# Kernel tuning notes

Measured on AMD Instinct MI355X. Metric: run time of the kernel, lower is better.

The kernel has to match this reference:

```python
import math
import jax, jax.numpy as jnp
import numpy as np

B, L, DIM, HEADS = 4, 2048, 1024, 8
HEAD = DIM // HEADS  # 128
SCALE_BASE = 512.0
EPS = 1e-5  # nn.GroupNorm default


def _xpos(x, downscale=False):
    # x: (..., L, dh). Faithful port of the RetNet XPOS (Jamie-Stirling impl).
    l, dh = x.shape[-2], x.shape[-1]
    half = dh // 2
    pos = jnp.arange(l, dtype=x.dtype)
    base = (jnp.arange(0, dh, 2, dtype=x.dtype) + 0.4 * dh) / (1.4 * dh)  # (half,)
    scale = base[None, :] ** (pos[:, None] / SCALE_BASE)                  # (L, half)
    inv_freq = 1.0 / (10000.0 ** (jnp.arange(half, dtype=x.dtype) / half))
    sinusoid = pos[:, None] * inv_freq[None, :]                           # (L, half)
    sin, cos = jnp.sin(sinusoid), jnp.cos(sinusoid)
    if downscale:
        scale = 1.0 / scale
    s = jnp.repeat(sin * scale, 2, axis=-1)  # duplicate_interleave -> (L, dh)
    c = jnp.repeat(cos * scale, 2, axis=-1)
    x1, x2 = x[..., ::2], x[..., 1::2]
    rot = jnp.stack([-x2, x1], axis=-1).reshape(x.shape)  # rotate_every_two
    return x * c + rot * s


def _decay_mask(l, gammas):
    # D[h, n, m] = gamma_h ** (n - m) for n >= m else 0
    n = jnp.arange(l)[:, None]
    m = jnp.arange(l)[None, :]
    lg = jnp.log(gammas)  # (h,)
    expo = (n - m).astype(jnp.float32)[None, :, :] * lg[:, None, None]
    return jnp.where((n >= m)[None], jnp.exp(expo), 0.0)  # (h, L, L)


def setup_inputs() -> dict:
    key = jax.random.key(0)
    ks = jax.random.split(key, 6)
    d = DIM
    return {
        "X": jax.random.normal(ks[0], (B, L, DIM), dtype=jnp.float32),
        "W_Q": jax.random.normal(ks[1], (HEADS, DIM, HEAD), dtype=jnp.float32) / d,
        "W_K": jax.random.normal(ks[2], (HEADS, DIM, HEAD), dtype=jnp.float32) / d,
        "W_V": jax.random.normal(ks[3], (HEADS, DIM, HEAD), dtype=jnp.float32) / d,
        "W_G": jax.random.normal(ks[4], (DIM, DIM), dtype=jnp.float32) / d,
        "W_O": jax.random.normal(ks[5], (DIM, DIM), dtype=jnp.float32) / d,
        "gn_weight": jnp.ones((DIM,), dtype=jnp.float32),
        "gn_bias": jnp.zeros((DIM,), dtype=jnp.float32),
    }


def reference(X, W_Q, W_K, W_V, W_G, W_O, gn_weight, gn_bias):
    b, l, d = X.shape
    h = W_Q.shape[0]
    # gammas = 1 - exp(linspace(log 1/32, log 1/512, heads))
    gammas = 1.0 - jnp.exp(jnp.linspace(math.log(1.0 / 32.0), math.log(1.0 / 512.0), h)).astype(jnp.float32)

    Q = jnp.einsum('bld,hde->bhle', X, W_Q)
    K = jnp.einsum('bld,hde->bhle', X, W_K)
    V = jnp.einsum('bld,hdv->bhlv', X, W_V)
    Q = _xpos(Q)
    K = _xpos(K, downscale=True)

    D = _decay_mask(l, gammas).astype(X.dtype)           # (h, L, L)
    scores = jnp.einsum('bhle,bhme->bhlm', Q, K) * D[None]
    Y = jnp.einsum('bhlm,bhmv->bhlv', scores, V)          # (b, h, L, head_v)

    # GroupNorm(heads, V) on rows of shape (V,): normalize per head group
    mean = Y.mean(axis=-1, keepdims=True)
    var = Y.var(axis=-1, keepdims=True)
    Yn = (Y - mean) * jax.lax.rsqrt(var + EPS)
    Yn = jnp.transpose(Yn, (0, 2, 1, 3)).reshape(b, l, -1)  # concat heads -> (b, L, V)
    Yn = Yn * gn_weight + gn_bias

    G = X @ W_G
    out = (G * jax.nn.sigmoid(G) * Yn) @ W_O  # swish gate then output proj
    return out
```

## Files before the change

kernel.cpp:

```cpp
#include <hip/hip_runtime.h>
#include <cmath>

#define BB 4
#define LL 2048
#define DD 1024
#define HH 8
#define MM (BB * LL)

struct Gammas { float lg2[8]; };
struct MMArgs { const ushort* Bt[4]; void* C[4]; void* C2[4]; int emode[4]; };

typedef __attribute__((ext_vector_type(8))) short bf16x8;
typedef __attribute__((ext_vector_type(4))) float f32x4;

__device__ __forceinline__ ushort f2bf(float f) {
    uint u = __builtin_bit_cast(uint, f);
    uint r = (u + 0x7fffu + ((u >> 16) & 1u)) >> 16;
    return (ushort)r;
}
__device__ __forceinline__ float bf2f(ushort h) {
    uint u = ((uint)h) << 16;
    return __builtin_bit_cast(float, u);
}
__device__ __forceinline__ void gload16(const void* g, void* l) {
    __builtin_amdgcn_global_load_lds((const __attribute__((address_space(1))) void*)g,
                                     (__attribute__((address_space(3))) void*)l, 16, 0, 0);
}

__global__ void xpos_table_kernel(float4* __restrict__ tbl) {
    int tid = blockIdx.x * blockDim.x + threadIdx.x;
    if (tid >= LL * 64) return;
    int l = tid >> 6, i = tid & 63;
    float inv = powf(10000.0f, -(float)i / 64.0f);
    float ang = (float)l * inv;
    float s = sinf(ang), c = cosf(ang);
    float base = (2.0f * (float)i + 51.2f) / 179.2f;
    float sc = powf(base, (float)l / 512.0f);
    tbl[tid] = make_float4(c * sc, s * sc, c / sc, s / sc);
}

__global__ __launch_bounds__(256) void cast_kernel(const float* __restrict__ X,
                                                   ushort* __restrict__ Xb) {
    int i = (blockIdx.x * 256 + threadIdx.x) * 4;
    float4 v = *(const float4*)&X[i];
    ushort4 o;
    o.x = f2bf(v.x); o.y = f2bf(v.y); o.z = f2bf(v.z); o.w = f2bf(v.w);
    *(ushort4*)&Xb[i] = o;
}

__global__ __launch_bounds__(256) void wtrans_kernel(const float* __restrict__ W,
                                                     ushort* __restrict__ Wt, int perhead) {
    __shared__ float T[64][68];
    const int k0 = blockIdx.y * 64, n0 = blockIdx.x * 64;
    const int t = threadIdx.x;
    for (int f = t; f < 64 * 16; f += 256) {
        int kk = f >> 4, s = f & 15;
        int n = n0 + s * 4;
        size_t src = perhead ? (size_t)(n >> 7) * 131072 + (size_t)(k0 + kk) * 128 + (n & 127)
                             : (size_t)(k0 + kk) * 1024 + n;
        *(float4*)&T[kk][s * 4] = *(const float4*)&W[src];
    }
    __syncthreads();
    for (int f = t; f < 64 * 8; f += 256) {
        int n = f >> 3, s = f & 7;
        __align__(16) ushort tmp[8];
        #pragma unroll
        for (int j = 0; j < 8; j++) tmp[j] = f2bf(T[s * 8 + j][n]);
        *(uint4*)&Wt[(size_t)(n0 + n) * 1024 + k0 + s * 8] = *(uint4*)tmp;
    }
}

__global__ __launch_bounds__(256, 4) void mm_kernel(
    const ushort* __restrict__ A, MMArgs args, const float4* __restrict__ tbl)
{
    __shared__ __align__(16) ushort As[2][128 * 32];
    __shared__ __align__(16) ushort Bs[2][128 * 32];
    const int t = threadIdx.x;
    const int w = t >> 6, lane = t & 63;
    const int ln = lane & 15, quad = lane >> 4;
    const int which = blockIdx.x >> 3;
    const ushort* Bt = args.Bt[which];
    void* Cv = args.C[which];
    void* Cv2 = args.C2[which];
    const int emode = args.emode[which];
    const int n0 = (blockIdx.x & 7) * 128, m0 = blockIdx.y * 128;
    const int wm = w & 1, wn = w >> 1;

    f32x4 acc[4][4];
    const f32x4 fzero = {0.f, 0.f, 0.f, 0.f};
    #pragma unroll
    for (int i = 0; i < 4; i++)
        #pragma unroll
        for (int j = 0; j < 4; j++) acc[i][j] = fzero;

    const int srow = w * 32 + (lane >> 2);
    const int scol = (lane & 3) * 8;
    const ushort* ga  = A  + (size_t)(m0 + srow) * 1024 + scol;
    const ushort* ga2 = ga + 16 * 1024;
    const ushort* gb  = Bt + (size_t)(n0 + srow) * 1024 + scol;
    const ushort* gb2 = gb + 16 * 1024;
    const int lo1 = (w * 32) * 32;
    const int lo2 = (w * 32 + 16) * 32;

    gload16(ga, &As[0][lo1]);
    gload16(ga2, &As[0][lo2]);
    gload16(gb, &Bs[0][lo1]);
    gload16(gb2, &Bs[0][lo2]);
    __syncthreads();

    for (int kt = 0; kt < 1024; kt += 32) {
        const int cur = (kt >> 5) & 1;
        if (kt < 1024 - 32) {
            const int nk = kt + 32;
            gload16(ga + nk, &As[cur ^ 1][lo1]);
            gload16(ga2 + nk, &As[cur ^ 1][lo2]);
            gload16(gb + nk, &Bs[cur ^ 1][lo1]);
            gload16(gb2 + nk, &Bs[cur ^ 1][lo2]);
        }
        bf16x8 am[4], bn[4];
        #pragma unroll
        for (int i = 0; i < 4; i++)
            am[i] = *(const bf16x8*)&As[cur][(wm * 64 + i * 16 + ln) * 32 + quad * 8];
        #pragma unroll
        for (int i = 0; i < 4; i++)
            bn[i] = *(const bf16x8*)&Bs[cur][(wn * 64 + i * 16 + ln) * 32 + quad * 8];
        #pragma unroll
        for (int mi = 0; mi < 4; mi++)
            #pragma unroll
            for (int ni = 0; ni < 4; ni++)
                acc[mi][ni] = __builtin_amdgcn_mfma_f32_16x16x32_bf16(
                    am[mi], bn[ni], acc[mi][ni], 0, 0, 0);
        __syncthreads();
    }

    #pragma unroll
    for (int mi = 0; mi < 4; mi++) {
        #pragma unroll
        for (int ni = 0; ni < 4; ni++) {
            const int row0 = m0 + wm * 64 + mi * 16 + quad * 4;
            const int e = wn * 64 + ni * 16 + ln;
            const int col = n0 + e;
            if (emode == 5) {
                const int b = row0 >> 11, l0 = row0 & (LL - 1);
                ushort4 pk;
                pk.x = f2bf(acc[mi][ni][0]); pk.y = f2bf(acc[mi][ni][1]);
                pk.z = f2bf(acc[mi][ni][2]); pk.w = f2bf(acc[mi][ni][3]);
                *(ushort4*)&((ushort*)Cv)[((size_t)(b * 1024 + col)) * 2048 + l0] = pk;
                continue;
            }
            float vv[4];
            #pragma unroll
            for (int r = 0; r < 4; r++) {
                float v = acc[mi][ni][r];
                if (emode == 1 || emode == 2 || emode == 6) {
                    float4 tt = tbl[(size_t)((row0 + r) & (LL - 1)) * 64 + (e >> 1)];
                    float cc = (emode == 1) ? tt.x : tt.z;
                    float ss = (emode == 1) ? tt.y : tt.w;
                    float partner = __shfl_xor(v, 1);
                    float rot = (e & 1) ? partner : -partner;
                    v = v * cc + rot * ss;
                } else if (emode == 3) {
                    v = v / (1.0f + expf(-v));
                }
                vv[r] = v;
                if (emode == 4)
                    ((float*)Cv)[(size_t)(row0 + r) * 1024 + col] = v;
                else
                    ((ushort*)Cv)[(size_t)(row0 + r) * 1024 + col] = f2bf(v);
            }
            if (emode == 6) {
                const int b = row0 >> 11, l0 = row0 & (LL - 1);
                ushort4 pk;
                pk.x = f2bf(vv[0]); pk.y = f2bf(vv[1]);
                pk.z = f2bf(vv[2]); pk.w = f2bf(vv[3]);
                *(ushort4*)&((ushort*)Cv2)[((size_t)(b * 1024 + col)) * 2048 + l0] = pk;
            }
        }
    }
}

__global__ __launch_bounds__(256) void state_kernel(
    const ushort* __restrict__ Ktb, const ushort* __restrict__ Vt,
    ushort* __restrict__ Sb, Gammas gp)
{
    __shared__ __align__(16) ushort shbuf[2 * 128 * 72];
    ushort* Ktl = shbuf;
    ushort* Vwl = shbuf + 128 * 72;

    const int t = threadIdx.x;
    const int w = t >> 6, lane = t & 63, ln = lane & 15, quad = lane >> 4;
    const int c = blockIdx.x, bh = blockIdx.y;
    const int b = bh >> 3, h = bh & 7;
    const float lg2 = gp.lg2[h];
    const size_t tbase = ((size_t)b * 1024 + h * 128) * 2048 + (size_t)c * 64;

    const int sr = t >> 1, soff = (t & 1) * 32;
    #pragma unroll
    for (int j = 0; j < 4; j++)
        *(uint4*)&Ktl[sr * 72 + soff + j * 8] =
            *(const uint4*)&Ktb[tbase + (size_t)sr * 2048 + soff + j * 8];
    #pragma unroll
    for (int j = 0; j < 4; j++) {
        uint4 raw = *(const uint4*)&Vt[tbase + (size_t)sr * 2048 + soff + j * 8];
        ushort* rp = (ushort*)&raw;
        __align__(16) ushort tmp[8];
        #pragma unroll
        for (int jj = 0; jj < 8; jj++) {
            int m = soff + j * 8 + jj;
            tmp[jj] = f2bf(bf2f(rp[jj]) * exp2f(lg2 * (float)(63 - m)));
        }
        *(uint4*)&Vwl[sr * 72 + soff + j * 8] = *(uint4*)tmp;
    }
    __syncthreads();

    const int wm = w & 1, wn = w >> 1;
    f32x4 acc[4][4];
    const f32x4 fzero = {0.f, 0.f, 0.f, 0.f};
    #pragma unroll
    for (int i = 0; i < 4; i++)
        #pragma unroll
        for (int j = 0; j < 4; j++) acc[i][j] = fzero;

    #pragma unroll
    for (int ks = 0; ks < 2; ks++) {
        bf16x8 am[4], bn[4];
        #pragma unroll
        for (int mi = 0; mi < 4; mi++)
            am[mi] = *(const bf16x8*)&Ktl[(wm * 64 + mi * 16 + ln) * 72 + ks * 32 + quad * 8];
        #pragma unroll
        for (int ni = 0; ni < 4; ni++)
            bn[ni] = *(const bf16x8*)&Vwl[(wn * 64 + ni * 16 + ln) * 72 + ks * 32 + quad * 8];
        #pragma unroll
        for (int mi = 0; mi < 4; mi++)
            #pragma unroll
            for (int ni = 0; ni < 4; ni++)
                acc[mi][ni] = __builtin_amdgcn_mfma_f32_16x16x32_bf16(
                    am[mi], bn[ni], acc[mi][ni], 0, 0, 0);
    }
    __syncthreads();

    ushort* Lsh = shbuf;
    #pragma unroll
    for (int mi = 0; mi < 4; mi++) {
        #pragma unroll
        for (int ni = 0; ni < 4; ni++) {
            const int d0 = wm * 64 + mi * 16 + quad * 4;
            const int v = wn * 64 + ni * 16 + ln;
            ushort4 pk;
            pk.x = f2bf(acc[mi][ni][0]); pk.y = f2bf(acc[mi][ni][1]);
            pk.z = f2bf(acc[mi][ni][2]); pk.w = f2bf(acc[mi][ni][3]);
            *(ushort4*)&Lsh[v * 136 + d0] = pk;
        }
    }
    __syncthreads();
    ushort* dst = Sb + (size_t)(bh * 32 + c) * 128 * 128;
    const int orow = t >> 1, ooff = (t & 1) * 64;
    #pragma unroll
    for (int j = 0; j < 8; j++)
        *(uint4*)&dst[(size_t)orow * 128 + ooff + j * 8] =
            *(uint4*)&Lsh[orow * 136 + ooff + j * 8];
}

__global__ __launch_bounds__(256) void scan_kernel(ushort* __restrict__ Sb, Gammas gp)
{
    const int t = threadIdx.x;
    const int vb = blockIdx.x, bh = blockIdx.y;
    const int h = bh & 7;
    const float g64 = exp2f(64.0f * gp.lg2[h]);
    const int v = vb * 16 + (t >> 4);
    const int d0 = (t & 15) * 8;

    float acc[8];
    #pragma unroll
    for (int j = 0; j < 8; j++) acc[j] = 0.f;

    for (int c = 1; c < 32; c++) {
        ushort* p = Sb + ((size_t)(bh * 32 + (c - 1)) * 128 + v) * 128 + d0;
        uint4 lv = *(const uint4*)p;
        ushort* lp = (ushort*)&lv;
        __align__(16) ushort o[8];
        #pragma unroll
        for (int j = 0; j < 8; j++) {
            acc[j] = g64 * acc[j] + bf2f(lp[j]);
            o[j] = f2bf(acc[j]);
        }
        *(uint4*)p = *(uint4*)o;
    }
}

__global__ __launch_bounds__(256) void ret2_kernel(
    const ushort* __restrict__ Qb, const ushort* __restrict__ Kb,
    const ushort* __restrict__ Vt, const ushort* __restrict__ Pt,
    const ushort* __restrict__ Gb,
    const float* __restrict__ gnw, const float* __restrict__ gnb,
    ushort* __restrict__ Z, Gammas gp)
{
    __shared__ __align__(16) ushort Ks[64 * 136];
    __shared__ __align__(16) ushort Vs[128 * 72];
    __shared__ __align__(16) ushort Ss[64 * 72];
    __shared__ __align__(16) ushort Ps[128 * 136];

    const int t = threadIdx.x;
    const int w = t >> 6, lane = t & 63, ln = lane & 15, quad = lane >> 4;
    const int c = blockIdx.x, bh = blockIdx.y;
    const int b = bh >> 3, h = bh & 7;
    const float lg2 = gp.lg2[h];
    const size_t qkbase = (size_t)b * LL * 1024 + (size_t)h * 128;
    const size_t vtbase = ((size_t)b * 1024 + h * 128) * 2048;
    const int n0 = c * 64;

    float dmk[4], drr[4];
    #pragma unroll
    for (int kt = 0; kt < 4; kt++)
        dmk[kt] = exp2f(-(float)(kt * 16 + quad * 4) * lg2);
    #pragma unroll
    for (int r = 0; r < 4; r++)
        drr[r] = exp2f(-(float)r * lg2);

    float gwv[8], gbv[8];
    #pragma unroll
    for (int vt = 0; vt < 8; vt++) {
        gwv[vt] = gnw[h * 128 + vt * 16 + ln];
        gbv[vt] = gnb[h * 128 + vt * 16 + ln];
    }

    const int krow = t >> 4, kc = (t & 15) * 8;
    const int vrow = t >> 3, vc = (t & 7) * 8;
    #pragma unroll
    for (int i = 0; i < 4; i++)
        *(uint4*)&Ks[(krow + i * 16) * 136 + kc] =
            *(const uint4*)&Kb[qkbase + (size_t)(n0 + krow + i * 16) * 1024 + kc];
    #pragma unroll
    for (int i = 0; i < 4; i++)
        *(uint4*)&Vs[(vrow + i * 32) * 72 + vc] =
            *(const uint4*)&Vt[vtbase + (size_t)(vrow + i * 32) * 2048 + n0 + vc];
    if (c > 0) {
        const ushort* psrc = Pt + (size_t)(bh * 32 + (c - 1)) * 128 * 128;
        const int pr = t >> 1, poff = (t & 1) * 64;
        #pragma unroll
        for (int j = 0; j < 8; j++)
            *(uint4*)&Ps[pr * 136 + poff + j * 8] =
                *(const uint4*)&psrc[(size_t)pr * 128 + poff + j * 8];
    }

    bf16x8 aq[4];
    #pragma unroll
    for (int ks = 0; ks < 4; ks++)
        aq[ks] = *(const bf16x8*)&Qb[qkbase + (size_t)(n0 + 16 * w + ln) * 1024
                                     + ks * 32 + quad * 8];
    f32x4 y[8];
    const f32x4 fzero = {0.f, 0.f, 0.f, 0.f};
    #pragma unroll
    for (int vt = 0; vt < 8; vt++) y[vt] = fzero;

    __syncthreads();

    if (c > 0) {
        #pragma unroll
        for (int ks = 0; ks < 4; ks++) {
            #pragma unroll
            for (int vt = 0; vt < 8; vt++) {
                bf16x8 bp = *(const bf16x8*)&Ps[(vt * 16 + ln) * 136 + ks * 32 + quad * 8];
                y[vt] = __builtin_amdgcn_mfma_f32_16x16x32_bf16(aq[ks], bp, y[vt], 0, 0, 0);
            }
        }
        #pragma unroll
        for (int rr = 0; rr < 4; rr++) {
            const float sc = exp2f(lg2 * (float)(16 * w + quad * 4 + rr + 1));
            #pragma unroll
            for (int vt = 0; vt < 8; vt++) y[vt][rr] *= sc;
        }
    }

    f32x4 s4[4];
    #pragma unroll
    for (int kt = 0; kt < 4; kt++) s4[kt] = fzero;
    #pragma unroll
    for (int ks = 0; ks < 4; ks++) {
        #pragma unroll
        for (int kt = 0; kt < 4; kt++) {
            bf16x8 bk = *(const bf16x8*)&Ks[(kt * 16 + ln) * 136 + ks * 32 + quad * 8];
            s4[kt] = __builtin_amdgcn_mfma_f32_16x16x32_bf16(bk, aq[ks], s4[kt], 0, 0, 0);
        }
    }
    const float dq = exp2f((float)(16 * w + ln) * lg2);
    #pragma unroll
    for (int kt = 0; kt < 4; kt++) {
        const float db = dq * dmk[kt];
        ushort4 pk;
        pk.x = f2bf((kt * 16 + quad * 4 + 0 <= 16 * w + ln) ? s4[kt][0] * db * drr[0] : 0.f);
        pk.y = f2bf((kt * 16 + quad * 4 + 1 <= 16 * w + ln) ? s4[kt][1] * db * drr[1] : 0.f);
        pk.z = f2bf((kt * 16 + quad * 4 + 2 <= 16 * w + ln) ? s4[kt][2] * db * drr[2] : 0.f);
        pk.w = f2bf((kt * 16 + quad * 4 + 3 <= 16 * w + ln) ? s4[kt][3] * db * drr[3] : 0.f);
        *(ushort4*)&Ss[(16 * w + ln) * 72 + kt * 16 + quad * 4] = pk;
    }
    #pragma unroll
    for (int ks2 = 0; ks2 < 2; ks2++) {
        bf16x8 as = *(const bf16x8*)&Ss[(16 * w + ln) * 72 + ks2 * 32 + quad * 8];
        #pragma unroll
        for (int vt = 0; vt < 8; vt++) {
            bf16x8 bv = *(const bf16x8*)&Vs[(vt * 16 + ln) * 72 + ks2 * 32 + quad * 8];
            y[vt] = __builtin_amdgcn_mfma_f32_16x16x32_bf16(as, bv, y[vt], 0, 0, 0);
        }
    }

    #pragma unroll
    for (int r = 0; r < 4; r++) {
        float s = 0.f, sq = 0.f;
        #pragma unroll
        for (int vt = 0; vt < 8; vt++) {
            float v = y[vt][r];
            s += v; sq += v * v;
        }
        #pragma unroll
        for (int off = 8; off >= 1; off >>= 1) {
            s  += __shfl_xor(s, off, 64);
            sq += __shfl_xor(sq, off, 64);
        }
        float mean = s * 0.0078125f;
        float var = sq * 0.0078125f - mean * mean;
        float rstd = rsqrtf(var + 1e-5f);
        const size_t row = (size_t)(b * LL + n0 + 16 * w + quad * 4 + r);
        #pragma unroll
        for (int vt = 0; vt < 8; vt++) {
            float gv = bf2f(Gb[row * 1024 + h * 128 + vt * 16 + ln]);
            float o = (y[vt][r] - mean) * rstd * gwv[vt] + gbv[vt];
            Z[row * 1024 + h * 128 + vt * 16 + ln] = f2bf(o * gv);
        }
    }
}

extern "C" void kernel_launch(void* const* d_in, const int* in_sizes, int n_in,
                              void* d_out, int out_size, void* d_ws, size_t ws_size,
                              hipStream_t stream) {
    const float* X   = (const float*)d_in[0];
    const float* Wq  = (const float*)d_in[1];
    const float* Wk  = (const float*)d_in[2];
    const float* Wv  = (const float*)d_in[3];
    const float* Wg  = (const float*)d_in[4];
    const float* Wo  = (const float*)d_in[5];
    const float* gnw = (const float*)d_in[6];
    const float* gnb = (const float*)d_in[7];
    float* out = (float*)d_out;

    const size_t MB = 1u << 20;
    char* base = (char*)d_ws;
    ushort* Sb  = (ushort*)base;
    float4* tbl = (float4*)base;
    ushort* Xb  = (ushort*)(base + 2 * MB);
    ushort* Wqt = (ushort*)(base + 18 * MB);
    ushort* Wkt = (ushort*)(base + 20 * MB);
    ushort* Wvt = (ushort*)(base + 22 * MB);
    ushort* Wgt = (ushort*)(base + 24 * MB);
    ushort* Wot = (ushort*)(base + 32 * MB);
    ushort* Qb  = (ushort*)(base + 34 * MB);
    ushort* Kb  = (ushort*)(base + 50 * MB);
    ushort* Gb  = (ushort*)(base + 66 * MB);
    ushort* Vt  = (ushort*)(base + 82 * MB);
    ushort* Ktb = (ushort*)(base + 98 * MB);
    ushort* Zb  = (ushort*)(base + 98 * MB);

    Gammas gp;
    for (int h = 0; h < 8; h++) {
        double lin = log(1.0 / 32.0) +
                     (log(1.0 / 512.0) - log(1.0 / 32.0)) * (double)h / 7.0;
        float gamma = 1.0f - expf((float)lin);
        gp.lg2[h] = log2f(gamma);
    }

    xpos_table_kernel<<<(LL * 64) / 256, 256, 0, stream>>>(tbl);
    cast_kernel<<<MM * 1024 / 1024, 256, 0, stream>>>(X, Xb);

    dim3 wgrid(16, 16);
    wtrans_kernel<<<wgrid, 256, 0, stream>>>(Wq, Wqt, 1);
    wtrans_kernel<<<wgrid, 256, 0, stream>>>(Wk, Wkt, 1);
    wtrans_kernel<<<wgrid, 256, 0, stream>>>(Wv, Wvt, 1);
    wtrans_kernel<<<wgrid, 256, 0, stream>>>(Wg, Wgt, 0);
    wtrans_kernel<<<wgrid, 256, 0, stream>>>(Wo, Wot, 0);

    MMArgs qa;
    qa.Bt[0] = Wqt; qa.Bt[1] = Wkt; qa.Bt[2] = Wvt; qa.Bt[3] = Wgt;
    qa.C[0] = Qb;   qa.C[1] = Kb;   qa.C[2] = Vt;   qa.C[3] = Gb;
    qa.C2[0] = nullptr; qa.C2[1] = Ktb; qa.C2[2] = nullptr; qa.C2[3] = nullptr;
    qa.emode[0] = 1; qa.emode[1] = 6; qa.emode[2] = 5; qa.emode[3] = 3;
    mm_kernel<<<dim3(32, 64), 256, 0, stream>>>(Xb, qa, tbl);

    state_kernel<<<dim3(32, 32), 256, 0, stream>>>(Ktb, Vt, Sb, gp);
    scan_kernel<<<dim3(8, 32), 256, 0, stream>>>(Sb, gp);
    ret2_kernel<<<dim3(32, 32), 256, 0, stream>>>(Qb, Kb, Vt, Sb, Gb,
                                                  gnw, gnb, Zb, gp);

    MMArgs oa;
    oa.Bt[0] = Wot; oa.Bt[1] = Wot; oa.Bt[2] = Wot; oa.Bt[3] = Wot;
    oa.C[0] = out;  oa.C[1] = out;  oa.C[2] = out;  oa.C[3] = out;
    oa.C2[0] = nullptr; oa.C2[1] = nullptr; oa.C2[2] = nullptr; oa.C2[3] = nullptr;
    oa.emode[0] = 4; oa.emode[1] = 4; oa.emode[2] = 4; oa.emode[3] = 4;
    mm_kernel<<<dim3(8, 64), 256, 0, stream>>>(Zb, oa, tbl);
}
```

Before: 367.8 us.

## Merge prep kernels into one launch and read state matrix directly from global

```diff
diff --git a/kernel.cpp b/kernel.cpp
--- a/kernel.cpp
+++ b/kernel.cpp
@@ -9,6 +9,7 @@
 
 struct Gammas { float lg2[8]; };
 struct MMArgs { const ushort* Bt[4]; void* C[4]; void* C2[4]; int emode[4]; };
+struct PrepArgs { const float* W[5]; ushort* Wt[5]; int perhead[5]; };
 
 typedef __attribute__((ext_vector_type(8))) short bf16x8;
 typedef __attribute__((ext_vector_type(4))) float f32x4;
@@ -27,32 +28,40 @@
                                      (__attribute__((address_space(3))) void*)l, 16, 0, 0);
 }
 
-__global__ void xpos_table_kernel(float4* __restrict__ tbl) {
-    int tid = blockIdx.x * blockDim.x + threadIdx.x;
-    if (tid >= LL * 64) return;
-    int l = tid >> 6, i = tid & 63;
-    float inv = powf(10000.0f, -(float)i / 64.0f);
-    float ang = (float)l * inv;
-    float s = sinf(ang), c = cosf(ang);
-    float base = (2.0f * (float)i + 51.2f) / 179.2f;
-    float sc = powf(base, (float)l / 512.0f);
-    tbl[tid] = make_float4(c * sc, s * sc, c / sc, s / sc);
-}
-
-__global__ __launch_bounds__(256) void cast_kernel(const float* __restrict__ X,
-                                                   ushort* __restrict__ Xb) {
-    int i = (blockIdx.x * 256 + threadIdx.x) * 4;
-    float4 v = *(const float4*)&X[i];
-    ushort4 o;
-    o.x = f2bf(v.x); o.y = f2bf(v.y); o.z = f2bf(v.z); o.w = f2bf(v.w);
-    *(ushort4*)&Xb[i] = o;
-}
-
-__global__ __launch_bounds__(256) void wtrans_kernel(const float* __restrict__ W,
-                                                     ushort* __restrict__ Wt, int perhead) {
+__global__ __launch_bounds__(256) void prep_kernel(
+    const float* __restrict__ X, ushort* __restrict__ Xb,
+    float4* __restrict__ tbl, PrepArgs pa)
+{
     __shared__ float T[64][68];
-    const int k0 = blockIdx.y * 64, n0 = blockIdx.x * 64;
+    const int blk = blockIdx.x;
     const int t = threadIdx.x;
+
+    if (blk < 512) {
+        int tid = blk * 256 + t;
+        int l = tid >> 6, i = tid & 63;
+        float inv = powf(10000.0f, -(float)i / 64.0f);
+        float ang = (float)l * inv;
+        float s = sinf(ang), c = cosf(ang);
+        float base = (2.0f * (float)i + 51.2f) / 179.2f;
+        float sc = powf(base, (float)l / 512.0f);
+        tbl[tid] = make_float4(c * sc, s * sc, c / sc, s / sc);
+        return;
+    }
+    if (blk < 8704) {
+        int i = ((blk - 512) * 256 + t) * 4;
+        float4 v = *(const float4*)&X[i];
+        ushort4 o;
+        o.x = f2bf(v.x); o.y = f2bf(v.y); o.z = f2bf(v.z); o.w = f2bf(v.w);
+        *(ushort4*)&Xb[i] = o;
+        return;
+    }
+    const int wblk = blk - 8704;
+    const int widx = wblk >> 8;
+    const int sub = wblk & 255;
+    const float* W = pa.W[widx];
+    ushort* Wt = pa.Wt[widx];
+    const int perhead = pa.perhead[widx];
+    const int k0 = (sub >> 4) * 64, n0 = (sub & 15) * 64;
     for (int f = t; f < 64 * 16; f += 256) {
         int kk = f >> 4, s = f & 15;
         int n = n0 + s * 4;
@@ -298,7 +307,6 @@
     __shared__ __align__(16) ushort Ks[64 * 136];
     __shared__ __align__(16) ushort Vs[128 * 72];
     __shared__ __align__(16) ushort Ss[64 * 72];
-    __shared__ __align__(16) ushort Ps[128 * 136];
 
     const int t = threadIdx.x;
     const int w = t >> 6, lane = t & 63, ln = lane & 15, quad = lane >> 4;
@@ -334,14 +342,6 @@
     for (int i = 0; i < 4; i++)
         *(uint4*)&Vs[(vrow + i * 32) * 72 + vc] =
             *(const uint4*)&Vt[vtbase + (size_t)(vrow + i * 32) * 2048 + n0 + vc];
-    if (c > 0) {
-        const ushort* psrc = Pt + (size_t)(bh * 32 + (c - 1)) * 128 * 128;
-        const int pr = t >> 1, poff = (t & 1) * 64;
-        #pragma unroll
-        for (int j = 0; j < 8; j++)
-            *(uint4*)&Ps[pr * 136 + poff + j * 8] =
-                *(const uint4*)&psrc[(size_t)pr * 128 + poff + j * 8];
-    }
 
     bf16x8 aq[4];
     #pragma unroll
@@ -353,16 +353,18 @@
     #pragma unroll
     for (int vt = 0; vt < 8; vt++) y[vt] = fzero;
 
-    __syncthreads();
-
     if (c > 0) {
+        const ushort* psrc = Pt + (size_t)(bh * 32 + (c - 1)) * 128 * 128;
         #pragma unroll
         for (int ks = 0; ks < 4; ks++) {
+            bf16x8 bp[8];
             #pragma unroll
-            for (int vt = 0; vt < 8; vt++) {
-                bf16x8 bp = *(const bf16x8*)&Ps[(vt * 16 + ln) * 136 + ks * 32 + quad * 8];
-                y[vt] = __builtin_amdgcn_mfma_f32_16x16x32_bf16(aq[ks], bp, y[vt], 0, 0, 0);
-            }
+            for (int vt = 0; vt < 8; vt++)
+                bp[vt] = *(const bf16x8*)&psrc[(size_t)(vt * 16 + ln) * 128
+                                               + ks * 32 + quad * 8];
+            #pragma unroll
+            for (int vt = 0; vt < 8; vt++)
+                y[vt] = __builtin_amdgcn_mfma_f32_16x16x32_bf16(aq[ks], bp[vt], y[vt], 0, 0, 0);
         }
         #pragma unroll
         for (int rr = 0; rr < 4; rr++) {
@@ -371,6 +373,8 @@
             for (int vt = 0; vt < 8; vt++) y[vt][rr] *= sc;
         }
     }
+
+    __syncthreads();
 
     f32x4 s4[4];
     #pragma unroll
@@ -468,15 +472,13 @@
         gp.lg2[h] = log2f(gamma);
     }
 
-    xpos_table_kernel<<<(LL * 64) / 256, 256, 0, stream>>>(tbl);
-    cast_kernel<<<MM * 1024 / 1024, 256, 0, stream>>>(X, Xb);
-
-    dim3 wgrid(16, 16);
-    wtrans_kernel<<<wgrid, 256, 0, stream>>>(Wq, Wqt, 1);
-    wtrans_kernel<<<wgrid, 256, 0, stream>>>(Wk, Wkt, 1);
-    wtrans_kernel<<<wgrid, 256, 0, stream>>>(Wv, Wvt, 1);
-    wtrans_kernel<<<wgrid, 256, 0, stream>>>(Wg, Wgt, 0);
-    wtrans_kernel<<<wgrid, 256, 0, stream>>>(Wo, Wot, 0);
+    PrepArgs pa;
+    pa.W[0] = Wq;  pa.Wt[0] = Wqt; pa.perhead[0] = 1;
+    pa.W[1] = Wk;  pa.Wt[1] = Wkt; pa.perhead[1] = 1;
+    pa.W[2] = Wv;  pa.Wt[2] = Wvt; pa.perhead[2] = 1;
+    pa.W[3] = Wg;  pa.Wt[3] = Wgt; pa.perhead[3] = 0;
+    pa.W[4] = Wo;  pa.Wt[4] = Wot; pa.perhead[4] = 0;
+    prep_kernel<<<9984, 256, 0, stream>>>(X, Xb, tbl, pa);
 
     MMArgs qa;
     qa.Bt[0] = Wqt; qa.Bt[1] = Wkt; qa.Bt[2] = Wvt; qa.Bt[3] = Wgt;
```

Result: faster. 354.5 us (median of 2 runs) (-3.6%).
